# Performance work log

Hardware: AMD Instinct MI355X
Metric: run time of the kernel (lower is better)

## Reference

```python
import jax, jax.numpy as jnp
import numpy as np

F_SIZE = 1000   # feature_size
FIELDS = 39     # field_size
K = 40          # ffm embedding dim
BATCH = 4096
LAYERS = [1024, 512, 256]


def setup_inputs() -> dict:
    key = jax.random.key(0)
    ks = jax.random.split(key, 12)
    inp = {
        "X": jax.random.normal(ks[0], (BATCH, F_SIZE), dtype=jnp.float32),
        "w1": jax.random.normal(ks[1], (F_SIZE,), dtype=jnp.float32) * 0.01,
        "b": jnp.full((1,), 0.5, dtype=jnp.float32),
        "nfk": jax.random.normal(ks[2], (F_SIZE, FIELDS, K), dtype=jnp.float32) * 0.01,
        "f2f": jax.random.randint(ks[3], (F_SIZE,), 0, FIELDS, dtype=jnp.int32),
    }
    dims = [F_SIZE] + LAYERS
    for i in range(len(LAYERS)):
        fan_in, fan_out = dims[i], dims[i + 1]
        scale = np.sqrt(6.0 / (fan_in + fan_out)).astype(np.float32)
        inp[f"deepW{i}"] = jax.random.uniform(ks[4 + i], (fan_in, fan_out), dtype=jnp.float32, minval=-scale, maxval=scale)
        inp[f"deepB{i}"] = jnp.zeros((fan_out,), dtype=jnp.float32)
    scale = np.sqrt(6.0 / (LAYERS[-1] + 1)).astype(np.float32)
    inp["outW"] = jax.random.uniform(ks[10], (LAYERS[-1], 1), dtype=jnp.float32, minval=-scale, maxval=scale)
    inp["outB"] = jnp.zeros((1,), dtype=jnp.float32)
    return inp


def reference(X, w1, b, nfk, f2f, deepW0, deepB0, deepW1, deepB1, deepW2, deepB2, outW, outB):
    # --- linear term: sum_i w1[i]*X[:,i] + b ---
    linear = X @ w1 + b[0]                                  # [B]

    # --- field-aware interaction ---
    # A[i, j, :] = nfk[i, f2f[j], :]  (gather over fields)
    F = nfk.shape[0]
    A = nfk[jnp.arange(F)[:, None], f2f[None, :], :]        # [F, F, K]
    # S[i, j] = <nfk[i, f2f[j]], nfk[j, f2f[i]]> -- batch-independent scalar
    S = jnp.einsum('ijk,jik->ij', A, A)                     # [F, F]
    M = jnp.triu(S, 1)                                      # keep i < j pairs only
    # sum_{i<j} S[i,j] * X[:,i] * X[:,j]
    interaction = jnp.sum((X @ M) * X, axis=1)              # [B]

    # --- deep part (train=False: no dropout) ---
    h = jax.nn.relu(X @ deepW0 + deepB0)
    h = jax.nn.relu(h @ deepW1 + deepB1)
    h = jax.nn.relu(h @ deepW2 + deepB2)
    deep = (h @ outW + outB).reshape(-1)                    # [B]

    out_sum = linear + interaction + deep                   # logits [B]
    return out_sum
```

## Files before the change

### kernel.cpp

```cpp
#include <hip/hip_runtime.h>


#define BATCH   4096
#define FSZ     1000
#define NFIELDS 39
#define KDIM    40

typedef __attribute__((ext_vector_type(8))) short short8v;
typedef __attribute__((ext_vector_type(4))) float f32x4;

__device__ __forceinline__ short f2bf(float f) {
  unsigned u = __builtin_bit_cast(unsigned, f);
  u += 0x7fff + ((u >> 16) & 1);
  return (short)(u >> 16);
}

typedef const __attribute__((address_space(1))) unsigned int* gas_ptr;
typedef __attribute__((address_space(3))) unsigned int* las_ptr;
__device__ __forceinline__ void gload16(const void* g, void* l) {
  __builtin_amdgcn_global_load_lds((gas_ptr)g, (las_ptr)l, 16, 0, 0);
}

__device__ __forceinline__ void transp32(
    const float* __restrict__ in, short* __restrict__ out, int idx, int nx,
    int K_in, int N_in, int Kpad, float (*t)[33], int tid)
{
  int n0 = (idx % nx) * 32, k0 = (idx / nx) * 32;
  int tx = tid & 31, ty = tid >> 5;
  #pragma unroll
  for (int i = 0; i < 32; i += 8) {
    int k = k0 + ty + i, n = n0 + tx;
    t[ty + i][tx] = (k < K_in && n < N_in) ? in[(size_t)k * N_in + n] : 0.f;
  }
  __syncthreads();
  #pragma unroll
  for (int i = 0; i < 32; i += 8) {
    int n = n0 + ty + i, k = k0 + tx;
    if (n < N_in && k < Kpad) out[(size_t)n * Kpad + k] = f2bf(t[tx][ty + i]);
  }
}

__global__ __launch_bounds__(256) void prep_kernel(
    const float* __restrict__ X, const float* __restrict__ nfk,
    const int* __restrict__ f2f,
    const float* __restrict__ W0, const float* __restrict__ W1,
    const float* __restrict__ W2,
    short* __restrict__ Xb, short* __restrict__ B12,
    short* __restrict__ Wt1, short* __restrict__ Wt2)
{
  __shared__ float tbuf[32][33];
  const int bid = blockIdx.x, tid = threadIdx.x;
  if (bid < 4096) {
    int k = tid * 4;
    short4 o = make_short4(0, 0, 0, 0);
    if (k < FSZ) {
      float4 v = *(const float4*)(X + (size_t)bid * FSZ + k);
      o = make_short4(f2bf(v.x), f2bf(v.y), f2bf(v.z), f2bf(v.w));
    }
    *(short4*)(Xb + (size_t)bid * 1024 + k) = o;
  } else if (bid < 8192) {
    int idx = bid - 4096;
    int n = idx >> 2, k = (idx & 3) * 256 + tid;
    float s = 0.f;
    if (n < FSZ && k < FSZ && n > k) {
      int fn = f2f[n], fk = f2f[k];
      const float4* p = (const float4*)(nfk + ((size_t)k * NFIELDS + fn) * KDIM);
      const float4* q = (const float4*)(nfk + ((size_t)n * NFIELDS + fk) * KDIM);
      #pragma unroll
      for (int t = 0; t < KDIM / 4; ++t) {
        float4 a = p[t], b = q[t];
        s += a.x * b.x + a.y * b.y + a.z * b.z + a.w * b.w;
      }
    }
    B12[(size_t)n * 1024 + k] = f2bf(s);
  } else if (bid < 9216) {
    transp32(W0, B12 + 1024 * 1024, bid - 8192, 32, 1000, 1024, 1024, tbuf, tid);
  } else if (bid < 9728) {
    transp32(W1, Wt1, bid - 9216, 16, 1024, 512, 1024, tbuf, tid);
  } else {
    transp32(W2, Wt2, bid - 9728, 8, 512, 256, 512, tbuf, tid);
  }
}

template<int BM, int BN, int EPI>
__global__ __launch_bounds__(256) void gemm_mfma(
    const short* __restrict__ A, const short* __restrict__ Bt,
    const float* __restrict__ bias, void* __restrict__ Cout,
    int N, int K,
    const float* __restrict__ X, const float* __restrict__ w1,
    float* __restrict__ partial)
{
  constexpr int AM = BM / 32, AN = BN / 32;
  __shared__ __align__(16) short As[2][BM * 64];
  __shared__ __align__(16) short Bs[2][BN * 64];
  __shared__ float pbuf[2][BM];

  const int tid  = threadIdx.x;
  const int wid  = tid >> 6;
  const int lane = tid & 63;
  const int wr   = wid >> 1, wc = wid & 1;
  const int row0 = blockIdx.y * BM;
  const int col0 = blockIdx.x * BN;

  const int lr8   = lane >> 3;
  const int cbase = (lane & 7) * 16;

  f32x4 acc[AM][AN];
  #pragma unroll
  for (int m = 0; m < AM; ++m)
    #pragma unroll
    for (int n = 0; n < AN; ++n) acc[m][n] = (f32x4)(0.f);

  auto stage = [&](int p, int k0) {
    #pragma unroll
    for (int j = 0; j < BM / 32; ++j) {
      int i = j * 4 + wid;
      int r = i * 8 + lr8;
      int cb = cbase ^ ((r & 7) << 4);
      gload16((const char*)A + (((size_t)(row0 + r) * K + k0) << 1) + cb,
              (char*)&As[p][0] + i * 1024);
    }
    #pragma unroll
    for (int j = 0; j < BN / 32; ++j) {
      int i = j * 4 + wid;
      int r = i * 8 + lr8;
      int cb = cbase ^ ((r & 7) << 4);
      gload16((const char*)Bt + (((size_t)(col0 + r) * K + k0) << 1) + cb,
              (char*)&Bs[p][0] + i * 1024);
    }
  };

  auto compute = [&](int p) {
    #pragma unroll
    for (int kk = 0; kk < 2; ++kk) {
      const int cb = kk * 64 + (lane >> 4) * 16;
      short8v a[AM], b[AN];
      #pragma unroll
      for (int m = 0; m < AM; ++m) {
        int r = wr * (BM / 2) + m * 16 + (lane & 15);
        a[m] = *(const short8v*)((const char*)&As[p][0] + r * 128 + (cb ^ ((r & 7) << 4)));
      }
      #pragma unroll
      for (int n = 0; n < AN; ++n) {
        int r = wc * (BN / 2) + n * 16 + (lane & 15);
        b[n] = *(const short8v*)((const char*)&Bs[p][0] + r * 128 + (cb ^ ((r & 7) << 4)));
      }
      #pragma unroll
      for (int m = 0; m < AM; ++m)
        #pragma unroll
        for (int n = 0; n < AN; ++n)
          acc[m][n] = __builtin_amdgcn_mfma_f32_16x16x32_bf16(a[m], b[n], acc[m][n], 0, 0, 0);
    }
  };

  int nt = K >> 6;
  if (EPI == 0 && blockIdx.x < 8) {
    int need = ((int)blockIdx.x * 2) + 2;
    nt = nt < need ? nt : need;
  }

  stage(0, 0);
  __syncthreads();
  for (int t = 0; t < nt; ++t) {
    if (t + 1 < nt) stage((t + 1) & 1, (t + 1) << 6);
    compute(t & 1);
    __syncthreads();
  }

  const int cr = (lane >> 4) * 4;
  const int cc = lane & 15;

  if (EPI == 0) {
    if (blockIdx.x < 8) {
      float rsum[AM * 4];
      #pragma unroll
      for (int i = 0; i < AM * 4; ++i) rsum[i] = 0.f;
      #pragma unroll
      for (int m = 0; m < AM; ++m) {
        #pragma unroll
        for (int n = 0; n < AN; ++n) {
          int gc = col0 + wc * (BN / 2) + n * 16 + cc;
          bool ok = gc < FSZ;
          float w1v = ok ? w1[gc] : 0.f;
          #pragma unroll
          for (int r = 0; r < 4; ++r) {
            int gr = row0 + wr * (BM / 2) + m * 16 + cr + r;
            float xv = ok ? X[(size_t)gr * FSZ + gc] : 0.f;
            rsum[m * 4 + r] = fmaf(acc[m][n][r] + w1v, xv, rsum[m * 4 + r]);
          }
        }
      }
      #pragma unroll
      for (int mask = 1; mask < 16; mask <<= 1)
        #pragma unroll
        for (int i = 0; i < AM * 4; ++i)
          rsum[i] += __shfl_xor(rsum[i], mask, 64);
      if (cc == 0) {
        #pragma unroll
        for (int m = 0; m < AM; ++m)
          #pragma unroll
          for (int r = 0; r < 4; ++r)
            pbuf[wc][wr * (BM / 2) + m * 16 + cr + r] = rsum[m * 4 + r];
      }
      __syncthreads();
      if (tid < BM)
        partial[(size_t)(row0 + tid) * 8 + blockIdx.x] = pbuf[0][tid] + pbuf[1][tid];
    } else {
      #pragma unroll
      for (int m = 0; m < AM; ++m) {
        #pragma unroll
        for (int n = 0; n < AN; ++n) {
          int gc = col0 - 1024 + wc * (BN / 2) + n * 16 + cc;
          float bv = bias[gc];
          #pragma unroll
          for (int r = 0; r < 4; ++r) {
            int gr = row0 + wr * (BM / 2) + m * 16 + cr + r;
            float v = fmaxf(acc[m][n][r] + bv, 0.f);
            ((short*)Cout)[(size_t)gr * 1024 + gc] = f2bf(v);
          }
        }
      }
    }
  } else if (EPI == 1) {
    #pragma unroll
    for (int m = 0; m < AM; ++m) {
      #pragma unroll
      for (int n = 0; n < AN; ++n) {
        int gc = col0 + wc * (BN / 2) + n * 16 + cc;
        float bv = bias[gc];
        #pragma unroll
        for (int r = 0; r < 4; ++r) {
          int gr = row0 + wr * (BM / 2) + m * 16 + cr + r;
          float v = fmaxf(acc[m][n][r] + bv, 0.f);
          ((short*)Cout)[(size_t)gr * N + gc] = f2bf(v);
        }
      }
    }
  } else {
    float rsum[AM * 4];
    #pragma unroll
    for (int i = 0; i < AM * 4; ++i) rsum[i] = 0.f;
    #pragma unroll
    for (int m = 0; m < AM; ++m) {
      #pragma unroll
      for (int n = 0; n < AN; ++n) {
        int gc = col0 + wc * (BN / 2) + n * 16 + cc;
        float bv = bias[gc];
        float ow = w1[gc];
        #pragma unroll
        for (int r = 0; r < 4; ++r) {
          float v = fmaxf(acc[m][n][r] + bv, 0.f);
          rsum[m * 4 + r] = fmaf(v, ow, rsum[m * 4 + r]);
        }
      }
    }
    #pragma unroll
    for (int mask = 1; mask < 16; mask <<= 1)
      #pragma unroll
      for (int i = 0; i < AM * 4; ++i)
        rsum[i] += __shfl_xor(rsum[i], mask, 64);
    if (cc == 0) {
      #pragma unroll
      for (int m = 0; m < AM; ++m)
        #pragma unroll
        for (int r = 0; r < 4; ++r)
          pbuf[wc][wr * (BM / 2) + m * 16 + cr + r] = rsum[m * 4 + r];
    }
    __syncthreads();
    if (tid < BM)
      partial[(size_t)(row0 + tid) * 4 + blockIdx.x] = pbuf[0][tid] + pbuf[1][tid];
  }
}

__global__ __launch_bounds__(256) void finalize_kernel(
    const float* __restrict__ part, const float* __restrict__ part2,
    const float* __restrict__ bsc, const float* __restrict__ oB,
    float* __restrict__ out)
{
  int b = blockIdx.x * 256 + threadIdx.x;
  const float4* p = (const float4*)(part + (size_t)b * 8);
  float4 a = p[0], c = p[1];
  float4 d = *(const float4*)(part2 + (size_t)b * 4);
  out[b] = a.x + a.y + a.z + a.w + c.x + c.y + c.z + c.w
         + d.x + d.y + d.z + d.w + bsc[0] + oB[0];
}

extern "C" void kernel_launch(void* const* d_in, const int* in_sizes, int n_in,
                              void* d_out, int out_size, void* d_ws, size_t ws_size,
                              hipStream_t stream) {
  const float* X   = (const float*)d_in[0];
  const float* w1  = (const float*)d_in[1];
  const float* bsc = (const float*)d_in[2];
  const float* nfk = (const float*)d_in[3];
  const int*   f2f = (const int*)d_in[4];
  const float* W0  = (const float*)d_in[5];
  const float* B0  = (const float*)d_in[6];
  const float* W1  = (const float*)d_in[7];
  const float* B1  = (const float*)d_in[8];
  const float* W2  = (const float*)d_in[9];
  const float* B2  = (const float*)d_in[10];
  const float* oW  = (const float*)d_in[11];
  const float* oB  = (const float*)d_in[12];
  float* out = (float*)d_out;

  char* ws = (char*)d_ws;
  short* Xb    = (short*)(ws);
  short* B12   = (short*)(ws + 8388608);
  short* Wt1   = (short*)(ws + 12582912);
  short* Wt2   = (short*)(ws + 13631488);
  float* part  = (float*)(ws + 13893632);
  float* part2 = (float*)(ws + 14024704);
  short* h0    = (short*)(ws + 14680064);
  short* h1    = (short*)(ws + 23068672);

  prep_kernel<<<9856, 256, 0, stream>>>(X, nfk, f2f, W0, W1, W2,
                                        Xb, B12, Wt1, Wt2);
  gemm_mfma<128, 128, 0><<<dim3(16, 32), 256, 0, stream>>>(
      Xb, B12, B0, h0, 2048, 1024, X, w1, part);
  gemm_mfma<64, 128, 1><<<dim3(4, 64), 256, 0, stream>>>(
      h0, Wt1, B1, h1, 512, 1024, nullptr, nullptr, nullptr);
  gemm_mfma<64, 64, 3><<<dim3(4, 64), 256, 0, stream>>>(
      h1, Wt2, B2, nullptr, 256, 512, nullptr, oW, part2);
  finalize_kernel<<<16, 256, 0, stream>>>(part, part2, bsc, oB, out);
}
```

Baseline: 83.74 us.

## Fuse finalize into last GEMM, cache nfk rows in LDS, single-buffer GEMM tiles

Several changes land together. The interaction-matrix prep now uses one block per row n and stages that row's nfk slice in shared memory, which cuts the block count and the redundant global reads. The GEMM drops double buffering for a single LDS buffer with an explicit wait and barrier per k-step, which halves LDS use but no longer overlaps loads with MFMA work. The epilogue reads bf16 Xb instead of fp32 X, the finalize kernel is fused into the last GEMM (tile changed to 32x256 so each block covers the full output row), and the second GEMM's tile changes to 64x64. Reading Xb trades a small precision loss in the linear and interaction terms for less epilogue traffic.

```diff
diff --git a/kernel.cpp b/kernel.cpp
--- a/kernel.cpp
+++ b/kernel.cpp
@@ -13,6 +13,10 @@
   unsigned u = __builtin_bit_cast(unsigned, f);
   u += 0x7fff + ((u >> 16) & 1);
   return (short)(u >> 16);
+}
+__device__ __forceinline__ float bf2f(unsigned short h) {
+  unsigned u = (unsigned)h << 16;
+  return __builtin_bit_cast(float, u);
 }
 
 typedef const __attribute__((address_space(1))) unsigned int* gas_ptr;
@@ -49,6 +53,7 @@
     short* __restrict__ Wt1, short* __restrict__ Wt2)
 {
   __shared__ float tbuf[32][33];
+  __shared__ float C[NFIELDS * 44];
   const int bid = blockIdx.x, tid = threadIdx.x;
   if (bid < 4096) {
     int k = tid * 4;
@@ -58,27 +63,36 @@
       o = make_short4(f2bf(v.x), f2bf(v.y), f2bf(v.z), f2bf(v.w));
     }
     *(short4*)(Xb + (size_t)bid * 1024 + k) = o;
-  } else if (bid < 8192) {
-    int idx = bid - 4096;
-    int n = idx >> 2, k = (idx & 3) * 256 + tid;
-    float s = 0.f;
-    if (n < FSZ && k < FSZ && n > k) {
-      int fn = f2f[n], fk = f2f[k];
-      const float4* p = (const float4*)(nfk + ((size_t)k * NFIELDS + fn) * KDIM);
-      const float4* q = (const float4*)(nfk + ((size_t)n * NFIELDS + fk) * KDIM);
-      #pragma unroll
-      for (int t = 0; t < KDIM / 4; ++t) {
-        float4 a = p[t], b = q[t];
-        s += a.x * b.x + a.y * b.y + a.z * b.z + a.w * b.w;
-      }
-    }
-    B12[(size_t)n * 1024 + k] = f2bf(s);
-  } else if (bid < 9216) {
-    transp32(W0, B12 + 1024 * 1024, bid - 8192, 32, 1000, 1024, 1024, tbuf, tid);
-  } else if (bid < 9728) {
-    transp32(W1, Wt1, bid - 9216, 16, 1024, 512, 1024, tbuf, tid);
+  } else if (bid < 5120) {
+    int n = bid - 4096;
+    if (n < FSZ) {
+      for (int t = tid; t < NFIELDS * KDIM; t += 256)
+        C[(t / KDIM) * 44 + (t % KDIM)] = nfk[(size_t)n * (NFIELDS * KDIM) + t];
+    }
+    __syncthreads();
+    int fn = (n < FSZ) ? f2f[n] : 0;
+    #pragma unroll
+    for (int kk = 0; kk < 4; ++kk) {
+      int k = kk * 256 + tid;
+      float s = 0.f;
+      if (n < FSZ && k < n) {
+        int fk = f2f[k];
+        const float4* p = (const float4*)(nfk + ((size_t)k * NFIELDS + fn) * KDIM);
+        const float4* q = (const float4*)&C[fk * 44];
+        #pragma unroll
+        for (int t = 0; t < KDIM / 4; ++t) {
+          float4 a = p[t], b = q[t];
+          s += a.x * b.x + a.y * b.y + a.z * b.z + a.w * b.w;
+        }
+      }
+      B12[(size_t)n * 1024 + k] = f2bf(s);
+    }
+  } else if (bid < 6144) {
+    transp32(W0, B12 + 1024 * 1024, bid - 5120, 32, 1000, 1024, 1024, tbuf, tid);
+  } else if (bid < 6656) {
+    transp32(W1, Wt1, bid - 6144, 16, 1024, 512, 1024, tbuf, tid);
   } else {
-    transp32(W2, Wt2, bid - 9728, 8, 512, 256, 512, tbuf, tid);
+    transp32(W2, Wt2, bid - 6656, 8, 512, 256, 512, tbuf, tid);
   }
 }
 
@@ -87,12 +101,13 @@
     const short* __restrict__ A, const short* __restrict__ Bt,
     const float* __restrict__ bias, void* __restrict__ Cout,
     int N, int K,
-    const float* __restrict__ X, const float* __restrict__ w1,
-    float* __restrict__ partial)
+    const short* __restrict__ Xb, const float* __restrict__ w1,
+    float* __restrict__ partial,
+    const float* __restrict__ c1, const float* __restrict__ c2)
 {
   constexpr int AM = BM / 32, AN = BN / 32;
-  __shared__ __align__(16) short As[2][BM * 64];
-  __shared__ __align__(16) short Bs[2][BN * 64];
+  __shared__ __align__(16) short As[BM * 64];
+  __shared__ __align__(16) short Bs[BN * 64];
   __shared__ float pbuf[2][BM];
 
   const int tid  = threadIdx.x;
@@ -111,14 +126,14 @@
     #pragma unroll
     for (int n = 0; n < AN; ++n) acc[m][n] = (f32x4)(0.f);
 
-  auto stage = [&](int p, int k0) {
+  auto stage = [&](int k0) {
     #pragma unroll
     for (int j = 0; j < BM / 32; ++j) {
       int i = j * 4 + wid;
       int r = i * 8 + lr8;
       int cb = cbase ^ ((r & 7) << 4);
       gload16((const char*)A + (((size_t)(row0 + r) * K + k0) << 1) + cb,
-              (char*)&As[p][0] + i * 1024);
+              (char*)As + i * 1024);
     }
     #pragma unroll
     for (int j = 0; j < BN / 32; ++j) {
@@ -126,11 +141,11 @@
       int r = i * 8 + lr8;
       int cb = cbase ^ ((r & 7) << 4);
       gload16((const char*)Bt + (((size_t)(col0 + r) * K + k0) << 1) + cb,
-              (char*)&Bs[p][0] + i * 1024);
+              (char*)Bs + i * 1024);
     }
   };
 
-  auto compute = [&](int p) {
+  auto compute = [&]() {
     #pragma unroll
     for (int kk = 0; kk < 2; ++kk) {
       const int cb = kk * 64 + (lane >> 4) * 16;
@@ -138,12 +153,12 @@
       #pragma unroll
       for (int m = 0; m < AM; ++m) {
         int r = wr * (BM / 2) + m * 16 + (lane & 15);
-        a[m] = *(const short8v*)((const char*)&As[p][0] + r * 128 + (cb ^ ((r & 7) << 4)));
+        a[m] = *(const short8v*)((const char*)As + r * 128 + (cb ^ ((r & 7) << 4)));
       }
       #pragma unroll
       for (int n = 0; n < AN; ++n) {
         int r = wc * (BN / 2) + n * 16 + (lane & 15);
-        b[n] = *(const short8v*)((const char*)&Bs[p][0] + r * 128 + (cb ^ ((r & 7) << 4)));
+        b[n] = *(const short8v*)((const char*)Bs + r * 128 + (cb ^ ((r & 7) << 4)));
       }
       #pragma unroll
       for (int m = 0; m < AM; ++m)
@@ -159,12 +174,12 @@
     nt = nt < need ? nt : need;
   }
 
-  stage(0, 0);
-  __syncthreads();
   for (int t = 0; t < nt; ++t) {
-    if (t + 1 < nt) stage((t + 1) & 1, (t + 1) << 6);
-    compute(t & 1);
     __syncthreads();
+    stage(t << 6);
+    asm volatile("s_waitcnt vmcnt(0)" ::: "memory");
+    __syncthreads();
+    compute();
   }
 
   const int cr = (lane >> 4) * 4;
@@ -180,12 +195,11 @@
         #pragma unroll
         for (int n = 0; n < AN; ++n) {
           int gc = col0 + wc * (BN / 2) + n * 16 + cc;
-          bool ok = gc < FSZ;
-          float w1v = ok ? w1[gc] : 0.f;
+          float w1v = (gc < FSZ) ? w1[gc] : 0.f;
           #pragma unroll
           for (int r = 0; r < 4; ++r) {
             int gr = row0 + wr * (BM / 2) + m * 16 + cr + r;
-            float xv = ok ? X[(size_t)gr * FSZ + gc] : 0.f;
+            float xv = bf2f((unsigned short)Xb[(size_t)gr * 1024 + gc]);
             rsum[m * 4 + r] = fmaf(acc[m][n][r] + w1v, xv, rsum[m * 4 + r]);
           }
         }
@@ -267,22 +281,14 @@
           pbuf[wc][wr * (BM / 2) + m * 16 + cr + r] = rsum[m * 4 + r];
     }
     __syncthreads();
-    if (tid < BM)
-      partial[(size_t)(row0 + tid) * 4 + blockIdx.x] = pbuf[0][tid] + pbuf[1][tid];
-  }
-}
-
-__global__ __launch_bounds__(256) void finalize_kernel(
-    const float* __restrict__ part, const float* __restrict__ part2,
-    const float* __restrict__ bsc, const float* __restrict__ oB,
-    float* __restrict__ out)
-{
-  int b = blockIdx.x * 256 + threadIdx.x;
-  const float4* p = (const float4*)(part + (size_t)b * 8);
-  float4 a = p[0], c = p[1];
-  float4 d = *(const float4*)(part2 + (size_t)b * 4);
-  out[b] = a.x + a.y + a.z + a.w + c.x + c.y + c.z + c.w
-         + d.x + d.y + d.z + d.w + bsc[0] + oB[0];
+    if (tid < BM) {
+      int gr = row0 + tid;
+      const float4* pp = (const float4*)(partial + (size_t)gr * 8);
+      float4 u = pp[0], v = pp[1];
+      ((float*)Cout)[gr] = pbuf[0][tid] + pbuf[1][tid]
+          + u.x + u.y + u.z + u.w + v.x + v.y + v.z + v.w + c1[0] + c2[0];
+    }
+  }
 }
 
 extern "C" void kernel_launch(void* const* d_in, const int* in_sizes, int n_in,
@@ -304,22 +310,20 @@
   float* out = (float*)d_out;
 
   char* ws = (char*)d_ws;
-  short* Xb    = (short*)(ws);
-  short* B12   = (short*)(ws + 8388608);
-  short* Wt1   = (short*)(ws + 12582912);
-  short* Wt2   = (short*)(ws + 13631488);
-  float* part  = (float*)(ws + 13893632);
-  float* part2 = (float*)(ws + 14024704);
-  short* h0    = (short*)(ws + 14680064);
-  short* h1    = (short*)(ws + 23068672);
-
-  prep_kernel<<<9856, 256, 0, stream>>>(X, nfk, f2f, W0, W1, W2,
+  short* Xb   = (short*)(ws);
+  short* B12  = (short*)(ws + 8388608);
+  short* Wt1  = (short*)(ws + 12582912);
+  short* Wt2  = (short*)(ws + 13631488);
+  float* part = (float*)(ws + 13893632);
+  short* h0   = (short*)(ws + 14680064);
+  short* h1   = (short*)(ws + 23068672);
+
+  prep_kernel<<<6784, 256, 0, stream>>>(X, nfk, f2f, W0, W1, W2,
                                         Xb, B12, Wt1, Wt2);
   gemm_mfma<128, 128, 0><<<dim3(16, 32), 256, 0, stream>>>(
-      Xb, B12, B0, h0, 2048, 1024, X, w1, part);
-  gemm_mfma<64, 128, 1><<<dim3(4, 64), 256, 0, stream>>>(
-      h0, Wt1, B1, h1, 512, 1024, nullptr, nullptr, nullptr);
-  gemm_mfma<64, 64, 3><<<dim3(4, 64), 256, 0, stream>>>(
-      h1, Wt2, B2, nullptr, 256, 512, nullptr, oW, part2);
-  finalize_kernel<<<16, 256, 0, stream>>>(part, part2, bsc, oB, out);
-}
+      Xb, B12, B0, h0, 2048, 1024, Xb, w1, part, nullptr, nullptr);
+  gemm_mfma<64, 64, 1><<<dim3(8, 64), 256, 0, stream>>>(
+      h0, Wt1, B1, h1, 512, 1024, nullptr, nullptr, nullptr, nullptr, nullptr);
+  gemm_mfma<32, 256, 3><<<dim3(1, 128), 256, 0, stream>>>(
+      h1, Wt2, B2, out, 256, 512, nullptr, oW, part, bsc, oB);
+}
```

Result: faster. 79.86 us (-4.6%).
